# Optimization experiments

Measured on AMD Instinct MI355X. Metric: run time of the kernel, lower is better.

The kernel has to match this reference:

```python
import jax, jax.numpy as jnp
import numpy as np

K = 5        # up_kernel
SIG = 2      # scale_factor
PAD = K // 2

def _conv(x, w, b, pad):
    y = jax.lax.conv_general_dilated(
        x, w, window_strides=(1, 1), padding=[(pad, pad), (pad, pad)],
        dimension_numbers=('NCHW', 'OIHW', 'NCHW'))
    return y + b[None, :, None, None]

def setup_inputs() -> dict:
    key = jax.random.key(0)
    k1, k2, k3 = jax.random.split(key, 3)
    n, c, h, w = 4, 256, 64, 64
    comp_c = 64
    enc_out = K * K * 1 * SIG * SIG  # 100
    x = jax.random.normal(k1, (n, c, h, w), dtype=jnp.float32)
    w_comp = jax.random.normal(k2, (comp_c, c, 1, 1), dtype=jnp.float32) * (1.0 / np.sqrt(c))
    b_comp = jnp.zeros((comp_c,), dtype=jnp.float32)
    w_enc = jax.random.normal(k3, (enc_out, comp_c, 3, 3), dtype=jnp.float32) * 0.001
    b_enc = jnp.zeros((enc_out,), dtype=jnp.float32)
    return {"x": x, "w_comp": w_comp, "b_comp": b_comp, "w_enc": w_enc, "b_enc": b_enc}

def reference(x, w_comp, b_comp, w_enc, b_enc):
    n, c, h, w = x.shape
    # 1) channel compressor (1x1 conv) + content encoder (3x3 conv, pad 1)
    compressed = _conv(x, w_comp, b_comp, pad=0)
    mask = _conv(compressed, w_enc, b_enc, pad=1)        # [n, K*K*SIG*SIG, h, w]
    # 2) kernel_normalizer: pixel_shuffle(sigma) then softmax over K*K
    # torch pixel_shuffle channel layout: (K*K, SIG, SIG)
    mask = mask.reshape(n, K * K, SIG, SIG, h, w)
    mask = jax.nn.softmax(mask, axis=1)                   # softmax over kernel taps
    # 3) CARAFE reassembly: gather KxK window around each low-res source pixel
    xp = jnp.pad(x, ((0, 0), (0, 0), (PAD, PAD), (PAD, PAD)))
    # patches: [n, c, K*K, h, w]  (zero-padded borders)
    patches = jnp.stack(
        [xp[:, :, di:di + h, dj:dj + w] for di in range(K) for dj in range(K)],
        axis=2)
    # out[n,c,h*SIG+i, w*SIG+j] = sum_k patches[n,c,k,h,w] * mask[n,k,i,j,h,w]
    out = jnp.einsum('nkijhw,nckhw->nchiwj', mask, patches)
    return out.reshape(n, c, h * SIG, w * SIG)
```

## Files before the change

kernel.cpp:

```cpp
#include <hip/hip_runtime.h>

#define HW      4096
#define W_DIM   64
#define C_IN    256
#define NK      25
#define NQ      112

typedef __bf16 bf16x4 __attribute__((ext_vector_type(4)));
typedef __bf16 bf16x8 __attribute__((ext_vector_type(8)));
typedef float  f32x4  __attribute__((ext_vector_type(4)));
typedef float  f32x2  __attribute__((ext_vector_type(2)));

static __device__ __forceinline__ unsigned short f2bf(float f) {
    unsigned x = __float_as_uint(f);
    return (unsigned short)((x + 0x7fffu + ((x >> 16) & 1u)) >> 16);
}
static __device__ __forceinline__ float bflo2f(unsigned u) { return __uint_as_float(u << 16); }
static __device__ __forceinline__ float bfhi2f(unsigned u) { return __uint_as_float(u & 0xffff0000u); }

__global__ __launch_bounds__(256) void k_prep(const float* __restrict__ wenc,
                                              const float* __restrict__ wcomp,
                                              unsigned short* __restrict__ wtb,
                                              unsigned short* __restrict__ wct) {
    int idx = blockIdx.x * 256 + threadIdx.x;
    if (idx < 64512) {
        int c = idx & 63;
        int t2 = idx >> 6;
        int kq = t2 % NQ;
        int tap = t2 / NQ;
        float v = (kq < 100) ? wenc[(kq * 64 + c) * 9 + tap] : 0.0f;
        wtb[idx] = f2bf(v);
    } else if (idx < 80896) {
        int j = idx - 64512;
        wct[j] = f2bf(wcomp[j]);
    }
}

__global__ __launch_bounds__(256) void k_compress(const float* __restrict__ x,
        const unsigned short* __restrict__ wct, const float* __restrict__ bcomp,
        unsigned short* __restrict__ comp) {
    __shared__ unsigned short As[64 * 260];
    __shared__ unsigned short Bs[64 * 260];
    __shared__ float sbc[64];
    int n = blockIdx.y, p0 = blockIdx.x * 64;
    int tid = threadIdx.x, wv = tid >> 6, lane = tid & 63;
    int l15 = lane & 15, l4 = lane >> 4;
    if (tid < 64) sbc[tid] = bcomp[tid];

    const float* xp = x + (size_t)n * C_IN * HW + p0;
#pragma unroll
    for (int s = 0; s < 32; ++s) {
        int cp = s * 4 + wv;
        float a = xp[(size_t)(2 * cp) * HW + lane];
        float b = xp[(size_t)(2 * cp + 1) * HW + lane];
        unsigned pk = (unsigned)f2bf(a) | ((unsigned)f2bf(b) << 16);
        *(unsigned*)(As + lane * 260 + cp * 2) = pk;
    }
    const unsigned* wsrc = (const unsigned*)wct;
#pragma unroll
    for (int s = 0; s < 32; ++s) {
        int slot = s * 256 + tid;
        int cc = slot >> 7, c2 = slot & 127;
        *(unsigned*)(Bs + cc * 260 + c2 * 2) = wsrc[cc * 128 + c2];
    }
    __syncthreads();

    f32x4 acc[4];
#pragma unroll
    for (int nt = 0; nt < 4; ++nt) acc[nt] = (f32x4){0.f, 0.f, 0.f, 0.f};
#pragma unroll
    for (int ck = 0; ck < 8; ++ck) {
        int ko = ck * 32 + l4 * 8;
        bf16x4 alo = *(const bf16x4*)(As + (wv * 16 + l15) * 260 + ko);
        bf16x4 ahi = *(const bf16x4*)(As + (wv * 16 + l15) * 260 + ko + 4);
        bf16x8 af = __builtin_shufflevector(alo, ahi, 0, 1, 2, 3, 4, 5, 6, 7);
#pragma unroll
        for (int nt = 0; nt < 4; ++nt) {
            bf16x4 blo = *(const bf16x4*)(Bs + (nt * 16 + l15) * 260 + ko);
            bf16x4 bhi = *(const bf16x4*)(Bs + (nt * 16 + l15) * 260 + ko + 4);
            bf16x8 bfr = __builtin_shufflevector(blo, bhi, 0, 1, 2, 3, 4, 5, 6, 7);
            acc[nt] = __builtin_amdgcn_mfma_f32_16x16x32_bf16(af, bfr, acc[nt], 0, 0, 0);
        }
    }
    unsigned short* op = comp + ((size_t)n * HW + p0 + wv * 16 + l4 * 4) * 64;
#pragma unroll
    for (int reg = 0; reg < 4; ++reg)
#pragma unroll
        for (int nt = 0; nt < 4; ++nt) {
            int cc = nt * 16 + l15;
            op[(size_t)reg * 64 + cc] = f2bf(acc[nt][reg] + sbc[cc]);
        }
}

#define CREC    136
#define SB0     13600
#define BSTRIDE 15232
#define EPI_PAD 116
__global__ __launch_bounds__(256) void k_enc(
        const unsigned short* __restrict__ comp,
        const unsigned short* __restrict__ wtb,
        const float* __restrict__ benc,
        float* __restrict__ mask) {
    __shared__ __align__(16) unsigned char smem[SB0 + 2 * BSTRIDE];
    __shared__ float sbias[NQ];
    int n = blockIdx.y, tile = blockIdx.x;
    int h0 = (tile >> 3) * 8, w0 = (tile & 7) * 8;
    int tid = threadIdx.x, wv = tid >> 6, lane = tid & 63;
    int l15 = lane & 15, l4 = lane >> 4;
    if (tid < NQ) sbias[tid] = (tid < 100) ? benc[tid] : 0.0f;

    const uint4* csrc = (const uint4*)(comp + (size_t)n * HW * 64);
#pragma unroll
    for (int pass = 0; pass < 4; ++pass) {
        int s = pass * 256 + tid;
        if (s < 800) {
            int px = s >> 3, j = s & 7;
            int gh = h0 + px / 10 - 1, gw = w0 + px % 10 - 1;
            uint4 v = make_uint4(0u, 0u, 0u, 0u);
            if ((unsigned)gh < 64u && (unsigned)gw < 64u)
                v = csrc[(size_t)(gh * 64 + gw) * 8 + j];
            *(uint2*)(smem + px * CREC + j * 16)     = make_uint2(v.x, v.y);
            *(uint2*)(smem + px * CREC + j * 16 + 8) = make_uint2(v.z, v.w);
        }
    }
    {
        const uint4* bs = (const uint4*)wtb;
#pragma unroll
        for (int pass = 0; pass < 4; ++pass) {
            int s = pass * 256 + tid;
            if (s < 896) {
                uint4 v = bs[s];
                int kq = s >> 3, j = s & 7;
                *(uint2*)(smem + SB0 + kq * CREC + j * 16)     = make_uint2(v.x, v.y);
                *(uint2*)(smem + SB0 + kq * CREC + j * 16 + 8) = make_uint2(v.z, v.w);
            }
        }
    }
    uint4 pre[4];
    {
        const uint4* bs = (const uint4*)(wtb + (size_t)1 * NQ * 64);
#pragma unroll
        for (int pass = 0; pass < 4; ++pass) {
            int s = pass * 256 + tid;
            if (s < 896) pre[pass] = bs[s];
        }
    }

    f32x4 acc[7];
#pragma unroll
    for (int nt = 0; nt < 7; ++nt) acc[nt] = (f32x4){0.f, 0.f, 0.f, 0.f};
    int r_t = 2 * wv + (l15 >> 3), cl = l15 & 7;

    for (int tap = 0; tap < 9; ++tap) {
        __syncthreads();
        if (tap < 8) {
            unsigned char* nbuf = smem + SB0 + ((tap + 1) & 1) * BSTRIDE;
#pragma unroll
            for (int pass = 0; pass < 4; ++pass) {
                int s = pass * 256 + tid;
                if (s < 896) {
                    int kq = s >> 3, j = s & 7;
                    *(uint2*)(nbuf + kq * CREC + j * 16)     = make_uint2(pre[pass].x, pre[pass].y);
                    *(uint2*)(nbuf + kq * CREC + j * 16 + 8) = make_uint2(pre[pass].z, pre[pass].w);
                }
            }
            if (tap < 7) {
                const uint4* bs = (const uint4*)(wtb + (size_t)(tap + 2) * NQ * 64);
#pragma unroll
                for (int pass = 0; pass < 4; ++pass) {
                    int s = pass * 256 + tid;
                    if (s < 896) pre[pass] = bs[s];
                }
            }
        }
        int ti = tap / 3, tj = tap % 3;
        int apx = (r_t + ti) * 10 + cl + tj;
        const unsigned char* cbuf = smem + SB0 + (tap & 1) * BSTRIDE;
#pragma unroll
        for (int ck = 0; ck < 2; ++ck) {
            int ko = ck * 64 + l4 * 16;
            bf16x4 alo = *(const bf16x4*)(smem + apx * CREC + ko);
            bf16x4 ahi = *(const bf16x4*)(smem + apx * CREC + ko + 8);
            bf16x8 af = __builtin_shufflevector(alo, ahi, 0, 1, 2, 3, 4, 5, 6, 7);
#pragma unroll
            for (int nt = 0; nt < 7; ++nt) {
                bf16x4 blo = *(const bf16x4*)(cbuf + (nt * 16 + l15) * CREC + ko);
                bf16x4 bhi = *(const bf16x4*)(cbuf + (nt * 16 + l15) * CREC + ko + 8);
                bf16x8 bfr = __builtin_shufflevector(blo, bhi, 0, 1, 2, 3, 4, 5, 6, 7);
                acc[nt] = __builtin_amdgcn_mfma_f32_16x16x32_bf16(af, bfr, acc[nt], 0, 0, 0);
            }
        }
    }
    __syncthreads();

    float* smE = (float*)(smem + SB0) + (size_t)wv * 16 * EPI_PAD;
    float* maskn = mask + (size_t)n * HW * 100;
#pragma unroll
    for (int nt = 0; nt < 7; ++nt) {
        f32x4 v = acc[nt];
#pragma unroll
        for (int reg = 0; reg < 4; ++reg)
            smE[(l4 * 4 + reg) * EPI_PAD + nt * 16 + l15] = v[reg];
    }
    {
        int spx = lane >> 2, q = lane & 3;
        float* row = smE + spx * EPI_PAD;
        float v[NK], mx = -1e30f;
#pragma unroll
        for (int k = 0; k < NK; ++k) {
            v[k] = row[4 * k + q] + sbias[4 * k + q];
            mx = fmaxf(mx, v[k]);
        }
        float ssum = 0.f;
#pragma unroll
        for (int k = 0; k < NK; ++k) { v[k] = __expf(v[k] - mx); ssum += v[k]; }
        float inv = 1.0f / ssum;
#pragma unroll
        for (int k = 0; k < NK; ++k) row[4 * k + q] = v[k] * inv;
    }
#pragma unroll
    for (int i = 0; i < 7; ++i) {
        int idx = i * 64 + lane;
        if (idx < 400) {
            int spx = idx / 25, f4 = idx % 25;
            int rr = 2 * wv + (spx >> 3), cc2 = spx & 7;
            size_t p = (size_t)(h0 + rr) * 64 + (w0 + cc2);
            *(float4*)(maskn + p * 100 + f4 * 4) =
                *(const float4*)(smE + spx * EPI_PAD + f4 * 4);
        }
    }
}

#define XSTR 66
#define MSTR 108
__global__ __launch_bounds__(256, 3) void k_reassemble(const float* __restrict__ x,
        const float* __restrict__ mask, float* __restrict__ out) {
    __shared__ float xs[144 * XSTR];
    __shared__ unsigned short ms[64 * MSTR];
    int n = blockIdx.z, cg = blockIdx.y, tile = blockIdx.x;
    int h0 = (tile >> 3) * 8, w0 = (tile & 7) * 8;
    int c0 = cg * 64;
    int tid = threadIdx.x;

    const float* xb = x + ((size_t)n * C_IN + c0) * HW;
#pragma unroll
    for (int i = 0; i < 36; ++i) {
        int s = i * 256 + tid;
        int c = s / 144, px = s % 144;
        int r = px / 12, cl = px % 12;
        int gh = h0 - 2 + r, gw = w0 - 2 + cl;
        float v = 0.f;
        if ((unsigned)gh < 64u && (unsigned)gw < 64u)
            v = xb[(size_t)c * HW + gh * W_DIM + gw];
        xs[px * XSTR + c] = v;
    }
    const float* mp = mask + (size_t)n * HW * 100;
#pragma unroll
    for (int i = 0; i < 25; ++i) {
        int s = i * 256 + tid;
        int px = s / 100, kq = s % 100;
        int gp = (h0 + (px >> 3)) * W_DIM + w0 + (px & 7);
        ms[px * MSTR + kq] = f2bf(mp[(size_t)gp * 100 + kq]);
    }
    __syncthreads();

    int px = tid & 63, cgl = tid >> 6;
    int wx = px & 7, hy = px >> 3;
    int cbase = cgl * 16;
    f32x4 acc[16];
#pragma unroll
    for (int u = 0; u < 16; ++u) acc[u] = (f32x4){0.f, 0.f, 0.f, 0.f};
    const unsigned short* mrow = ms + px * MSTR;
#pragma unroll
    for (int di = 0; di < 5; ++di)
#pragma unroll
        for (int dj = 0; dj < 5; ++dj) {
            int t = di * 5 + dj;
            uint2 mw = *(const uint2*)(mrow + t * 4);
            f32x4 m4;
            m4[0] = bflo2f(mw.x); m4[1] = bfhi2f(mw.x);
            m4[2] = bflo2f(mw.y); m4[3] = bfhi2f(mw.y);
            const float* xrow = xs + ((hy + di) * 12 + wx + dj) * XSTR + cbase;
#pragma unroll
            for (int u2 = 0; u2 < 8; ++u2) {
                f32x2 xv = *(const f32x2*)(xrow + u2 * 2);
                acc[u2 * 2 + 0] += m4 * xv[0];
                acc[u2 * 2 + 1] += m4 * xv[1];
            }
        }
#pragma unroll
    for (int u = 0; u < 16; ++u) {
        float* ob = out + (((size_t)n * C_IN + c0 + cbase + u) * 128 + 2 * (h0 + hy)) * 128
                        + 2 * (w0 + wx);
        *(float2*)(ob)       = make_float2(acc[u][0], acc[u][1]);
        *(float2*)(ob + 128) = make_float2(acc[u][2], acc[u][3]);
    }
}

extern "C" void kernel_launch(void* const* d_in, const int* in_sizes, int n_in,
                              void* d_out, int out_size, void* d_ws, size_t ws_size,
                              hipStream_t stream) {
    const float* x      = (const float*)d_in[0];
    const float* w_comp = (const float*)d_in[1];
    const float* b_comp = (const float*)d_in[2];
    const float* w_enc  = (const float*)d_in[3];
    const float* b_enc  = (const float*)d_in[4];
    float* out = (float*)d_out;
    unsigned char* ws = (unsigned char*)d_ws;

    unsigned short* comp = (unsigned short*)(ws);
    unsigned short* wtb  = (unsigned short*)(ws + 2097152);
    unsigned short* wct  = (unsigned short*)(ws + 2226176);
    float*          maskp = (float*)(ws + 2258944);

    hipLaunchKernelGGL(k_prep,       dim3(316),      dim3(256), 0, stream,
                       w_enc, w_comp, wtb, wct);
    hipLaunchKernelGGL(k_compress,   dim3(64, 4),    dim3(256), 0, stream,
                       x, wct, b_comp, comp);
    hipLaunchKernelGGL(k_enc,        dim3(64, 4),    dim3(256), 0, stream,
                       comp, wtb, b_enc, maskp);
    hipLaunchKernelGGL(k_reassemble, dim3(64, 4, 4), dim3(256), 0, stream,
                       x, maskp, out);
}
```

Before: 142.8 us.

## Store softmax mask as bf16 and retile reassembly to 16-channel blocks

The encoder epilogue now writes the normalized mask in bf16 rather than fp32, which halves mask write and read traffic and removes the conversion step from the reassembly load. The reassembly kernel is retiled from 64 channels to 16 channels per block, with 4 channels per thread. This cuts accumulator registers and shared memory so more blocks fit per CU (launch bound 6). It also remaps a flat grid so consecutive blocks spread across spatial tiles and channel groups, and loads x with float2 and the mask with uint2. In exchange, each 5x5 mask tile is reloaded for every channel group (16 times instead of 4), and halo reuse per block drops.

```diff
diff --git a/kernel.cpp b/kernel.cpp
--- a/kernel.cpp
+++ b/kernel.cpp
@@ -100,7 +100,7 @@
         const unsigned short* __restrict__ comp,
         const unsigned short* __restrict__ wtb,
         const float* __restrict__ benc,
-        float* __restrict__ mask) {
+        unsigned short* __restrict__ mask) {
     __shared__ __align__(16) unsigned char smem[SB0 + 2 * BSTRIDE];
     __shared__ float sbias[NQ];
     int n = blockIdx.y, tile = blockIdx.x;
@@ -194,7 +194,7 @@
     __syncthreads();
 
     float* smE = (float*)(smem + SB0) + (size_t)wv * 16 * EPI_PAD;
-    float* maskn = mask + (size_t)n * HW * 100;
+    unsigned short* maskn = mask + (size_t)n * HW * 100;
 #pragma unroll
     for (int nt = 0; nt < 7; ++nt) {
         f32x4 v = acc[nt];
@@ -225,75 +225,78 @@
             int spx = idx / 25, f4 = idx % 25;
             int rr = 2 * wv + (spx >> 3), cc2 = spx & 7;
             size_t p = (size_t)(h0 + rr) * 64 + (w0 + cc2);
-            *(float4*)(maskn + p * 100 + f4 * 4) =
-                *(const float4*)(smE + spx * EPI_PAD + f4 * 4);
-        }
-    }
-}
-
-#define XSTR 66
-#define MSTR 108
-__global__ __launch_bounds__(256, 3) void k_reassemble(const float* __restrict__ x,
-        const float* __restrict__ mask, float* __restrict__ out) {
-    __shared__ float xs[144 * XSTR];
-    __shared__ unsigned short ms[64 * MSTR];
-    int n = blockIdx.z, cg = blockIdx.y, tile = blockIdx.x;
+            const float* sp = smE + spx * EPI_PAD + f4 * 4;
+            unsigned u0 = (unsigned)f2bf(sp[0]) | ((unsigned)f2bf(sp[1]) << 16);
+            unsigned u1 = (unsigned)f2bf(sp[2]) | ((unsigned)f2bf(sp[3]) << 16);
+            *(uint2*)(maskn + p * 100 + f4 * 4) = make_uint2(u0, u1);
+        }
+    }
+}
+
+#define XSTR2 20
+#define MSTR2 108
+__global__ __launch_bounds__(256, 6) void k_reassemble(const float* __restrict__ x,
+        const unsigned short* __restrict__ mask, float* __restrict__ out) {
+    __shared__ __align__(16) float xs[144 * XSTR2];
+    __shared__ __align__(16) unsigned short ms[64 * MSTR2];
+    int flat = blockIdx.x;
+    int nf = (flat & 7) * 512 + (flat >> 3);
+    int tile = nf & 63, cg = (nf >> 6) & 15, n = nf >> 10;
     int h0 = (tile >> 3) * 8, w0 = (tile & 7) * 8;
-    int c0 = cg * 64;
     int tid = threadIdx.x;
 
-    const float* xb = x + ((size_t)n * C_IN + c0) * HW;
-#pragma unroll
-    for (int i = 0; i < 36; ++i) {
+    const float* xb = x + ((size_t)n * C_IN + cg * 16) * HW;
+#pragma unroll
+    for (int i = 0; i < 5; ++i) {
         int s = i * 256 + tid;
-        int c = s / 144, px = s % 144;
-        int r = px / 12, cl = px % 12;
-        int gh = h0 - 2 + r, gw = w0 - 2 + cl;
-        float v = 0.f;
-        if ((unsigned)gh < 64u && (unsigned)gw < 64u)
-            v = xb[(size_t)c * HW + gh * W_DIM + gw];
-        xs[px * XSTR + c] = v;
-    }
-    const float* mp = mask + (size_t)n * HW * 100;
-#pragma unroll
-    for (int i = 0; i < 25; ++i) {
+        if (s < 1152) {
+            int c = s / 72, rem = s % 72;
+            int r = rem / 6, j = rem % 6;
+            int gh = h0 - 2 + r, gw = w0 - 2 + j * 2;
+            float2 v = make_float2(0.f, 0.f);
+            if ((unsigned)gh < 64u && (unsigned)gw < 64u)
+                v = *(const float2*)(xb + (size_t)c * HW + gh * W_DIM + gw);
+            int px = r * 12 + j * 2;
+            xs[px * XSTR2 + c]       = v.x;
+            xs[(px + 1) * XSTR2 + c] = v.y;
+        }
+    }
+    const unsigned short* mp = mask + (size_t)n * HW * 100;
+#pragma unroll
+    for (int i = 0; i < 7; ++i) {
         int s = i * 256 + tid;
-        int px = s / 100, kq = s % 100;
-        int gp = (h0 + (px >> 3)) * W_DIM + w0 + (px & 7);
-        ms[px * MSTR + kq] = f2bf(mp[(size_t)gp * 100 + kq]);
+        if (s < 1600) {
+            int px = s / 25, q = s % 25;
+            int gp = (h0 + (px >> 3)) * W_DIM + w0 + (px & 7);
+            *(uint2*)(ms + px * MSTR2 + q * 4) =
+                *(const uint2*)(mp + (size_t)gp * 100 + q * 4);
+        }
     }
     __syncthreads();
 
-    int px = tid & 63, cgl = tid >> 6;
+    int px = tid & 63, w = tid >> 6;
     int wx = px & 7, hy = px >> 3;
-    int cbase = cgl * 16;
-    f32x4 acc[16];
-#pragma unroll
-    for (int u = 0; u < 16; ++u) acc[u] = (f32x4){0.f, 0.f, 0.f, 0.f};
-    const unsigned short* mrow = ms + px * MSTR;
+    f32x4 acc0 = {0.f, 0.f, 0.f, 0.f}, acc1 = {0.f, 0.f, 0.f, 0.f};
+    f32x4 acc2 = {0.f, 0.f, 0.f, 0.f}, acc3 = {0.f, 0.f, 0.f, 0.f};
+    const unsigned short* mrow = ms + px * MSTR2;
 #pragma unroll
     for (int di = 0; di < 5; ++di)
 #pragma unroll
         for (int dj = 0; dj < 5; ++dj) {
             int t = di * 5 + dj;
             uint2 mw = *(const uint2*)(mrow + t * 4);
-            f32x4 m4;
-            m4[0] = bflo2f(mw.x); m4[1] = bfhi2f(mw.x);
-            m4[2] = bflo2f(mw.y); m4[3] = bfhi2f(mw.y);
-            const float* xrow = xs + ((hy + di) * 12 + wx + dj) * XSTR + cbase;
-#pragma unroll
-            for (int u2 = 0; u2 < 8; ++u2) {
-                f32x2 xv = *(const f32x2*)(xrow + u2 * 2);
-                acc[u2 * 2 + 0] += m4 * xv[0];
-                acc[u2 * 2 + 1] += m4 * xv[1];
-            }
-        }
-#pragma unroll
-    for (int u = 0; u < 16; ++u) {
-        float* ob = out + (((size_t)n * C_IN + c0 + cbase + u) * 128 + 2 * (h0 + hy)) * 128
+            f32x4 xv = *(const f32x4*)(xs + ((hy + di) * 12 + wx + dj) * XSTR2 + w * 4);
+            acc0 += xv * bflo2f(mw.x);
+            acc1 += xv * bfhi2f(mw.x);
+            acc2 += xv * bflo2f(mw.y);
+            acc3 += xv * bfhi2f(mw.y);
+        }
+#pragma unroll
+    for (int u = 0; u < 4; ++u) {
+        float* ob = out + (((size_t)n * C_IN + cg * 16 + w * 4 + u) * 128 + 2 * (h0 + hy)) * 128
                         + 2 * (w0 + wx);
-        *(float2*)(ob)       = make_float2(acc[u][0], acc[u][1]);
-        *(float2*)(ob + 128) = make_float2(acc[u][2], acc[u][3]);
+        *(float2*)(ob)       = make_float2(acc0[u], acc1[u]);
+        *(float2*)(ob + 128) = make_float2(acc2[u], acc3[u]);
     }
 }
 
@@ -308,10 +311,10 @@
     float* out = (float*)d_out;
     unsigned char* ws = (unsigned char*)d_ws;
 
-    unsigned short* comp = (unsigned short*)(ws);
-    unsigned short* wtb  = (unsigned short*)(ws + 2097152);
-    unsigned short* wct  = (unsigned short*)(ws + 2226176);
-    float*          maskp = (float*)(ws + 2258944);
+    unsigned short* comp  = (unsigned short*)(ws);
+    unsigned short* wtb   = (unsigned short*)(ws + 2097152);
+    unsigned short* wct   = (unsigned short*)(ws + 2226176);
+    unsigned short* maskp = (unsigned short*)(ws + 2258944);
 
     hipLaunchKernelGGL(k_prep,       dim3(316),      dim3(256), 0, stream,
                        w_enc, w_comp, wtb, wct);
@@ -319,6 +322,6 @@
                        x, wct, b_comp, comp);
     hipLaunchKernelGGL(k_enc,        dim3(64, 4),    dim3(256), 0, stream,
                        comp, wtb, b_enc, maskp);
-    hipLaunchKernelGGL(k_reassemble, dim3(64, 4, 4), dim3(256), 0, stream,
+    hipLaunchKernelGGL(k_reassemble, dim3(4096),     dim3(256), 0, stream,
                        x, maskp, out);
 }
```

After: 121.3 us. 1.18x faster.
